# Kernel optimization log

Measured on AMD Instinct MI355X. Metric: run time of the kernel, lower is better.

The kernel has to match this reference:

```python
import jax, jax.numpy as jnp
import numpy as np

B, T, C, H = 2, 2048, 1024, 16
D = C // H  # head dim = 64


def setup_inputs() -> dict:
    key = jax.random.key(0)
    ks = jax.random.split(key, 3)
    x = jax.random.normal(ks[0], (B, T, C), dtype=jnp.float32)
    W_attn = jax.random.normal(ks[1], (C, 3 * C), dtype=jnp.float32) * (1.0 / np.sqrt(C))
    b_attn = jnp.zeros((3 * C,), dtype=jnp.float32)
    W_proj = jax.random.normal(ks[2], (C, C), dtype=jnp.float32) * (1.0 / np.sqrt(C))
    b_proj = jnp.zeros((C,), dtype=jnp.float32)
    return {"x": x, "W_attn": W_attn, "b_attn": b_attn, "W_proj": W_proj, "b_proj": b_proj}


def reference(x, W_attn, b_attn, W_proj, b_proj):
    Bb, Tt, Cc = x.shape
    qkv = x @ W_attn + b_attn                       # [B,T,3C]
    q, k, v = jnp.split(qkv, 3, axis=-1)            # each [B,T,C]
    q = q.reshape(Bb, Tt, H, D).transpose(0, 2, 1, 3)  # [B,H,T,D]
    k = k.reshape(Bb, Tt, H, D).transpose(0, 2, 1, 3)
    v = v.reshape(Bb, Tt, H, D).transpose(0, 2, 1, 3)
    # NOTE: original scales by 1/sqrt(n_embd), not 1/sqrt(head_dim)
    scale = 1.0 / np.sqrt(Cc)
    wei = jnp.einsum('bhqd,bhkd->bhqk', q, k) * scale  # [B,H,T,T]
    causal = jnp.tril(jnp.ones((Tt, Tt), dtype=bool))
    wei = jnp.where(causal, wei, -jnp.inf)
    wei = jax.nn.softmax(wei, axis=-1)
    out = jnp.einsum('bhqk,bhkd->bhqd', wei, v)        # [B,H,T,D]
    out = out.transpose(0, 2, 1, 3).reshape(Bb, Tt, Cc)
    return out @ W_proj + b_proj
```

## Files before the change

kernel.cpp:

```cpp
#include <hip/hip_runtime.h>


typedef short bfrag __attribute__((ext_vector_type(8)));
typedef float facc  __attribute__((ext_vector_type(4)));
typedef float f16v  __attribute__((ext_vector_type(16)));
typedef float f4v   __attribute__((ext_vector_type(4)));
typedef unsigned int u32x2 __attribute__((ext_vector_type(2)));
typedef unsigned int u32x4v __attribute__((ext_vector_type(4)));
typedef unsigned short u16;

#define MFMA16(a, b, c) __builtin_amdgcn_mfma_f32_16x16x32_bf16((a), (b), (c), 0, 0, 0)
#define MFMA32(a, b, c) __builtin_amdgcn_mfma_f32_32x32x16_bf16((a), (b), (c), 0, 0, 0)

__device__ __forceinline__ u16 f2bf(float f) {
  union { float f; unsigned u; } v; v.f = f;
  unsigned r = v.u + 0x7fffu + ((v.u >> 16) & 1u);
  return (u16)(r >> 16);
}

__device__ __forceinline__ unsigned cvtpk(float lo, float hi) {
  unsigned r;
  asm("v_cvt_pk_bf16_f32 %0, %1, %2" : "=v"(r) : "v"(lo), "v"(hi));
  return r;
}

__device__ __forceinline__ void async_lds16(const void* g, void* l) {
  __builtin_amdgcn_global_load_lds(
      (const __attribute__((address_space(1))) unsigned char*)g,
      (__attribute__((address_space(3))) unsigned char*)l, 16, 0, 0);
}


__global__ void cast_bf16_kernel(const float* __restrict__ s, u16* __restrict__ d, int n) {
  int i = (blockIdx.x * blockDim.x + threadIdx.x) * 4;
  if (i >= n) return;
  f4v v = *reinterpret_cast<const f4v*>(s + i);
  u32x2 w;
  w[0] = (unsigned)f2bf(v[0]) | ((unsigned)f2bf(v[1]) << 16);
  w[1] = (unsigned)f2bf(v[2]) | ((unsigned)f2bf(v[3]) << 16);
  *reinterpret_cast<u32x2*>(d + i) = w;
}

__global__ void transpose_cast_kernel(const float* __restrict__ src, u16* __restrict__ dst,
                                      int K, int N) {
  __shared__ float tile[32][33];
  int tx = threadIdx.x, ty = threadIdx.y;
  int n0 = blockIdx.x * 32, k0 = blockIdx.y * 32;
  for (int j = ty; j < 32; j += 8)
    tile[j][tx] = src[(size_t)(k0 + j) * N + (n0 + tx)];
  __syncthreads();
  for (int j = ty; j < 32; j += 8)
    dst[(size_t)(n0 + j) * K + (k0 + tx)] = f2bf(tile[tx][j]);
}


template <int EPI>
__global__ __launch_bounds__(256) void gemm_kernel(
    const u16* __restrict__ A, const u16* __restrict__ Bt,
    const float* __restrict__ bias, float* __restrict__ outf,
    u16* __restrict__ qb, u16* __restrict__ kb, u16* __restrict__ vb) {
  constexpr int KD = 1024;
  __shared__ u16 As[128 * 32];
  __shared__ u16 Bs[128 * 32];
  const int t = threadIdx.x;
  const int l = t & 63, w = t >> 6;
  const int wm = w >> 1, wn = w & 1;
  const int lg = l >> 4, lc = l & 15;
  const int m0 = blockIdx.y * 128, n0 = blockIdx.x * 128;
  facc acc[4][4] = {};
  const int srow = t >> 2, scol = (t & 3) * 8;
  const u16* ga = A + (size_t)(m0 + srow) * KD + scol;
  const u16* gb = Bt + (size_t)(n0 + srow) * KD + scol;
  u16* la0 = As + t * 8;  u16* la1 = As + 2048 + t * 8;
  u16* lb0 = Bs + t * 8;  u16* lb1 = Bs + 2048 + t * 8;
  for (int kt = 0; kt < KD / 32; ++kt) {
    __syncthreads();
    async_lds16(ga + kt * 32, la0);
    async_lds16(ga + 64 * KD + kt * 32, la1);
    async_lds16(gb + kt * 32, lb0);
    async_lds16(gb + 64 * KD + kt * 32, lb1);
    __syncthreads();
    bfrag a[4], b[4];
#pragma unroll
    for (int mi = 0; mi < 4; ++mi)
      a[mi] = *reinterpret_cast<const bfrag*>(As + (wm * 64 + mi * 16 + lc) * 32 + lg * 8);
#pragma unroll
    for (int ni = 0; ni < 4; ++ni)
      b[ni] = *reinterpret_cast<const bfrag*>(Bs + (wn * 64 + ni * 16 + lc) * 32 + lg * 8);
#pragma unroll
    for (int mi = 0; mi < 4; ++mi)
#pragma unroll
      for (int ni = 0; ni < 4; ++ni)
        acc[mi][ni] = MFMA16(a[mi], b[ni], acc[mi][ni]);
  }
#pragma unroll
  for (int mi = 0; mi < 4; ++mi) {
#pragma unroll
    for (int ni = 0; ni < 4; ++ni) {
#pragma unroll
      for (int r = 0; r < 4; ++r) {
        int gm = m0 + wm * 64 + mi * 16 + lg * 4 + r;
        int gn = n0 + wn * 64 + ni * 16 + lc;
        float val = acc[mi][ni][r] + bias[gn];
        if constexpr (EPI == 0) {
          int sec = gn >> 10, ci = gn & 1023;
          int h = ci >> 6, d = ci & 63;
          int b_ = gm >> 11, tq = gm & 2047;
          int bh = b_ * 16 + h;
          if (sec == 0) {
            qb[((size_t)bh * 2048 + tq) * 64 + d] = f2bf(val * 0.045084439f);
          } else if (sec == 1) {
            kb[((size_t)bh * 2048 + tq) * 64 + d] = f2bf(val);
          } else {
            vb[((size_t)bh * 64 + d) * 2048 + tq] = f2bf(val);
          }
        } else {
          outf[(size_t)gm * 1024 + gn] = val;
        }
      }
    }
  }
}


__global__ __launch_bounds__(128, 2) void attn_kernel(
    const u16* __restrict__ Qb, const u16* __restrict__ Kb,
    const u16* __restrict__ Vtb, u16* __restrict__ attn) {
  constexpr int T = 2048;
  __shared__ u16 Ks[2][64 * 64];
  const int t = threadIdx.x;
  const int l = t & 63, w = t >> 6;
  const int c = l & 31, h = l >> 5;
  const int b = blockIdx.x;
  const int bh = b & 31;
  const int tile = 31 - (b >> 5);
  const int ntile = tile + 1;
  const size_t base = (size_t)bh * T * 64;
  const u16* Qp = Qb + base;
  const u16* Kp = Kb + base;
  const u16* Vp = Vtb + base;
  const int q0 = tile * 64 + w * 32;

  bfrag qf[4];
#pragma unroll
  for (int dt = 0; dt < 4; ++dt)
    qf[dt] = *reinterpret_cast<const bfrag*>(Qp + (size_t)(q0 + c) * 64 + dt * 16 + 8 * h);

  f16v o[2] = {};
  f16v s[2];
  float m_ = -1e30f, l_ = 0.f;

  const int srow = w * 32 + (l >> 3);
  const int sw8  = ((t & 7) ^ ((t >> 3) & 7)) * 8;
  const int loff = w * 2048 + l * 8;

#define STAGE_K(bufi, kvb_)                                                      \
  {                                                                              \
    _Pragma("unroll")                                                            \
    for (int j = 0; j < 4; ++j)                                                  \
      async_lds16(Kp + (size_t)((kvb_) + srow + 8 * j) * 64 + sw8,               \
                  &Ks[bufi][loff + 512 * j]);                                    \
  }

#define LOADV(vf, kvb_)                                                          \
  {                                                                              \
    _Pragma("unroll")                                                            \
    for (int nt = 0; nt < 2; ++nt)                                               \
      _Pragma("unroll")                                                          \
      for (int k2 = 0; k2 < 4; ++k2)                                             \
        vf[nt * 4 + k2] = *reinterpret_cast<const bfrag*>(                       \
            Vp + (size_t)(32 * nt + c) * T + (kvb_) + 16 * k2 + 8 * h);          \
  }

  auto qk = [&](const u16* ks) {
    const f16v z = {};
    s[0] = z; s[1] = z;
    __builtin_amdgcn_s_setprio(1);
#pragma unroll
    for (int kt = 0; kt < 2; ++kt)
#pragma unroll
      for (int dt = 0; dt < 4; ++dt) {
        const bfrag a = *reinterpret_cast<const bfrag*>(
            ks + (32 * kt + c) * 64 + (((2 * dt + h) ^ (c & 7)) * 8));
        s[kt] = MFMA32(a, qf[dt], s[kt]);
      }
    __builtin_amdgcn_s_setprio(0);
  };

  auto pv = [&](const bfrag pa[4], const bfrag vf[8]) {
    __builtin_amdgcn_s_setprio(1);
#pragma unroll
    for (int nt = 0; nt < 2; ++nt)
#pragma unroll
      for (int k2 = 0; k2 < 4; ++k2)
        o[nt] = MFMA32(pa[k2], vf[nt * 4 + k2], o[nt]);
    __builtin_amdgcn_s_setprio(0);
  };

  auto softmax_pa = [&](int it, bfrag pa[4]) {
    if (it == ntile - 1) {
      const int kvb = 64 * it;
      const int qq = q0 + c;
#pragma unroll
      for (int kt = 0; kt < 2; ++kt)
#pragma unroll
        for (int r = 0; r < 16; ++r) {
          const int kk = kvb + 32 * kt + (r & 3) + 8 * (r >> 2) + 4 * h;
          if (kk > qq) s[kt][r] = -1e30f;
        }
    }
    float pms[4] = {-1e30f, -1e30f, -1e30f, -1e30f};
#pragma unroll
    for (int kt = 0; kt < 2; ++kt)
#pragma unroll
      for (int r = 0; r < 16; ++r) pms[r & 3] = fmaxf(pms[r & 3], s[kt][r]);
    float pm = fmaxf(fmaxf(pms[0], pms[1]), fmaxf(pms[2], pms[3]));
    pm = fmaxf(pm, __shfl_xor(pm, 32));
    if (!__all(pm <= m_ + 8.0f)) {
      const float mn = fmaxf(m_, pm);
      const float al = exp2f(m_ - mn);
      l_ *= al;
#pragma unroll
      for (int r = 0; r < 16; ++r) {
        const float ar = __shfl(al, (r & 3) + 8 * (r >> 2) + 4 * h);
        o[0][r] *= ar;
        o[1][r] *= ar;
      }
      m_ = mn;
    }
    float ps[4] = {0.f, 0.f, 0.f, 0.f};
#pragma unroll
    for (int kt = 0; kt < 2; ++kt)
#pragma unroll
      for (int r = 0; r < 16; ++r) {
        const float e = exp2f(s[kt][r] - m_);
        s[kt][r] = e;
        ps[r & 3] += e;
      }
    float pss = (ps[0] + ps[1]) + (ps[2] + ps[3]);
    pss += __shfl_xor(pss, 32);
    l_ += pss;
#pragma unroll
    for (int kt = 0; kt < 2; ++kt)
#pragma unroll
      for (int sub = 0; sub < 2; ++sub) {
        const int bs = 8 * sub;
        unsigned x1 = cvtpk(s[kt][bs + 0], s[kt][bs + 1]);
        unsigned y1 = cvtpk(s[kt][bs + 4], s[kt][bs + 5]);
        asm volatile("v_permlane32_swap_b32 %0, %1" : "+v"(x1), "+v"(y1));
        unsigned x2 = cvtpk(s[kt][bs + 2], s[kt][bs + 3]);
        unsigned y2 = cvtpk(s[kt][bs + 6], s[kt][bs + 7]);
        asm volatile("v_permlane32_swap_b32 %0, %1" : "+v"(x2), "+v"(y2));
        union { u32x4v wv; bfrag f; } u;
        u.wv[0] = x1; u.wv[1] = x2; u.wv[2] = y1; u.wv[3] = y2;
        pa[2 * kt + sub] = u.f;
      }
  };

  bfrag vfA[8], vfB[8], paA[4], paB[4];

  STAGE_K(0, 0);
  LOADV(vfA, 0);
  __syncthreads();
  if (ntile > 1) STAGE_K(1, 64);
  qk(Ks[0]);
  softmax_pa(0, paA);

  bool lastA = true;
  for (int it = 1; it < ntile; ) {
    __syncthreads();
    if (it + 1 < ntile) STAGE_K((it + 1) & 1, 64 * (it + 1));
    LOADV(vfB, 64 * it);
    qk(Ks[it & 1]);
    pv(paA, vfA);
    softmax_pa(it, paB);
    ++it; lastA = false;
    if (it >= ntile) break;
    __syncthreads();
    if (it + 1 < ntile) STAGE_K((it + 1) & 1, 64 * (it + 1));
    LOADV(vfA, 64 * it);
    qk(Ks[it & 1]);
    pv(paB, vfB);
    softmax_pa(it, paA);
    ++it; lastA = true;
  }
  if (lastA) pv(paA, vfA); else pv(paB, vfB);

  const int b_ = bh >> 4, hd = bh & 15;
  const float linv = 1.0f / l_;
#pragma unroll
  for (int r = 0; r < 16; ++r) {
    const int row = (r & 3) + 8 * (r >> 2) + 4 * h;
    const float lr = __shfl(linv, row);
    const int tq = q0 + row;
#pragma unroll
    for (int nt = 0; nt < 2; ++nt) {
      const int col = hd * 64 + 32 * nt + c;
      attn[((size_t)(b_ * T + tq)) * 1024 + col] = f2bf(o[nt][r] * lr);
    }
  }
#undef STAGE_K
#undef LOADV
}


extern "C" void kernel_launch(void* const* d_in, const int* in_sizes, int n_in,
                              void* d_out, int out_size, void* d_ws, size_t ws_size,
                              hipStream_t stream) {
  const float* x      = (const float*)d_in[0];
  const float* W_attn = (const float*)d_in[1];
  const float* b_attn = (const float*)d_in[2];
  const float* W_proj = (const float*)d_in[3];
  const float* b_proj = (const float*)d_in[4];
  float* out = (float*)d_out;
  char* ws = (char*)d_ws;
  u16* xb   = (u16*)(ws);
  u16* Wat  = (u16*)(ws + (8u  << 20));
  u16* Wpt  = (u16*)(ws + (14u << 20));
  u16* Qb   = (u16*)(ws + (16u << 20));
  u16* Kb   = (u16*)(ws + (24u << 20));
  u16* Vtb  = (u16*)(ws + (32u << 20));
  u16* attn = (u16*)(ws + (40u << 20));

  cast_bf16_kernel<<<4096, 256, 0, stream>>>(x, xb, 4096 * 1024);
  transpose_cast_kernel<<<dim3(96, 32), dim3(32, 8), 0, stream>>>(W_attn, Wat, 1024, 3072);
  transpose_cast_kernel<<<dim3(32, 32), dim3(32, 8), 0, stream>>>(W_proj, Wpt, 1024, 1024);
  gemm_kernel<0><<<dim3(24, 32), 256, 0, stream>>>(xb, Wat, b_attn, nullptr, Qb, Kb, Vtb);
  attn_kernel<<<1024, 128, 0, stream>>>(Qb, Kb, Vtb, attn);
  gemm_kernel<1><<<dim3(8, 32), 256, 0, stream>>>(attn, Wpt, b_proj, out, nullptr, nullptr, nullptr);
}
```

Baseline: 138.8 us.

## Use single-wave attention blocks loading K directly into registers without LDS

The attention kernel now launches one 64-thread wave per block, each covering 32 query rows, instead of two waves sharing a 64-row tile. K fragments are loaded straight from global memory into registers and prefetched one iteration ahead, replacing the double-buffered async LDS staging and its __syncthreads barriers. This removes LDS traffic and block synchronisation and doubles the number of blocks for scheduling. In exchange, K reuse between the two waves of a tile is lost, so K is read from global or L2 twice as often, and register pressure grows from holding K fragments.

After: 158.4 us. 1.14x slower.

```diff
diff --git a/kernel.cpp b/kernel.cpp
--- a/kernel.cpp
+++ b/kernel.cpp
@@ -123,23 +123,21 @@
 }
 
 
-__global__ __launch_bounds__(128, 2) void attn_kernel(
+__global__ __launch_bounds__(64, 2) void attn_kernel(
     const u16* __restrict__ Qb, const u16* __restrict__ Kb,
     const u16* __restrict__ Vtb, u16* __restrict__ attn) {
   constexpr int T = 2048;
-  __shared__ u16 Ks[2][64 * 64];
-  const int t = threadIdx.x;
-  const int l = t & 63, w = t >> 6;
+  const int l = threadIdx.x & 63;
   const int c = l & 31, h = l >> 5;
   const int b = blockIdx.x;
   const int bh = b & 31;
-  const int tile = 31 - (b >> 5);
-  const int ntile = tile + 1;
+  const int chunk = 63 - (b >> 5);
+  const int ntile = (chunk >> 1) + 1;
+  const int q0 = chunk * 32;
   const size_t base = (size_t)bh * T * 64;
   const u16* Qp = Qb + base;
   const u16* Kp = Kb + base;
   const u16* Vp = Vtb + base;
-  const int q0 = tile * 64 + w * 32;
 
   bfrag qf[4];
 #pragma unroll
@@ -150,18 +148,15 @@
   f16v s[2];
   float m_ = -1e30f, l_ = 0.f;
 
-  const int srow = w * 32 + (l >> 3);
-  const int sw8  = ((t & 7) ^ ((t >> 3) & 7)) * 8;
-  const int loff = w * 2048 + l * 8;
-
-#define STAGE_K(bufi, kvb_)                                                      \
+#define LOADK(kf, kvb_)                                                          \
   {                                                                              \
     _Pragma("unroll")                                                            \
-    for (int j = 0; j < 4; ++j)                                                  \
-      async_lds16(Kp + (size_t)((kvb_) + srow + 8 * j) * 64 + sw8,               \
-                  &Ks[bufi][loff + 512 * j]);                                    \
-  }
-
+    for (int kt = 0; kt < 2; ++kt)                                               \
+      _Pragma("unroll")                                                          \
+      for (int dt = 0; dt < 4; ++dt)                                             \
+        kf[kt * 4 + dt] = *reinterpret_cast<const bfrag*>(                       \
+            Kp + (size_t)((kvb_) + 32 * kt + c) * 64 + 16 * dt + 8 * h);         \
+  }
 #define LOADV(vf, kvb_)                                                          \
   {                                                                              \
     _Pragma("unroll")                                                            \
@@ -172,18 +167,15 @@
             Vp + (size_t)(32 * nt + c) * T + (kvb_) + 16 * k2 + 8 * h);          \
   }
 
-  auto qk = [&](const u16* ks) {
+  auto qk = [&](const bfrag kf[8]) {
     const f16v z = {};
     s[0] = z; s[1] = z;
     __builtin_amdgcn_s_setprio(1);
 #pragma unroll
     for (int kt = 0; kt < 2; ++kt)
 #pragma unroll
-      for (int dt = 0; dt < 4; ++dt) {
-        const bfrag a = *reinterpret_cast<const bfrag*>(
-            ks + (32 * kt + c) * 64 + (((2 * dt + h) ^ (c & 7)) * 8));
-        s[kt] = MFMA32(a, qf[dt], s[kt]);
-      }
+      for (int dt = 0; dt < 4; ++dt)
+        s[kt] = MFMA32(kf[kt * 4 + dt], qf[dt], s[kt]);
     __builtin_amdgcn_s_setprio(0);
   };
 
@@ -257,34 +249,27 @@
       }
   };
 
-  bfrag vfA[8], vfB[8], paA[4], paB[4];
-
-  STAGE_K(0, 0);
+  bfrag kf[8], vfA[8], vfB[8], pa[4];
+
+  LOADK(kf, 0);
   LOADV(vfA, 0);
-  __syncthreads();
-  if (ntile > 1) STAGE_K(1, 64);
-  qk(Ks[0]);
-  softmax_pa(0, paA);
-
-  bool lastA = true;
-  for (int it = 1; it < ntile; ) {
-    __syncthreads();
-    if (it + 1 < ntile) STAGE_K((it + 1) & 1, 64 * (it + 1));
-    LOADV(vfB, 64 * it);
-    qk(Ks[it & 1]);
-    pv(paA, vfA);
-    softmax_pa(it, paB);
-    ++it; lastA = false;
-    if (it >= ntile) break;
-    __syncthreads();
-    if (it + 1 < ntile) STAGE_K((it + 1) & 1, 64 * (it + 1));
-    LOADV(vfA, 64 * it);
-    qk(Ks[it & 1]);
-    pv(paB, vfB);
-    softmax_pa(it, paA);
-    ++it; lastA = true;
-  }
-  if (lastA) pv(paA, vfA); else pv(paB, vfB);
+
+  int it = 0;
+  bool useA = true;
+  while (true) {
+    qk(kf);
+    if (it + 1 < ntile) LOADK(kf, 64 * (it + 1));
+    softmax_pa(it, pa);
+    if (useA) {
+      if (it + 1 < ntile) LOADV(vfB, 64 * (it + 1));
+      pv(pa, vfA);
+    } else {
+      if (it + 1 < ntile) LOADV(vfA, 64 * (it + 1));
+      pv(pa, vfB);
+    }
+    useA = !useA;
+    if (++it >= ntile) break;
+  }
 
   const int b_ = bh >> 4, hd = bh & 15;
   const float linv = 1.0f / l_;
@@ -299,7 +284,7 @@
       attn[((size_t)(b_ * T + tq)) * 1024 + col] = f2bf(o[nt][r] * lr);
     }
   }
-#undef STAGE_K
+#undef LOADK
 #undef LOADV
 }
 
@@ -326,6 +311,6 @@
   transpose_cast_kernel<<<dim3(96, 32), dim3(32, 8), 0, stream>>>(W_attn, Wat, 1024, 3072);
   transpose_cast_kernel<<<dim3(32, 32), dim3(32, 8), 0, stream>>>(W_proj, Wpt, 1024, 1024);
   gemm_kernel<0><<<dim3(24, 32), 256, 0, stream>>>(xb, Wat, b_attn, nullptr, Qb, Kb, Vtb);
-  attn_kernel<<<1024, 128, 0, stream>>>(Qb, Kb, Vtb, attn);
+  attn_kernel<<<2048, 64, 0, stream>>>(Qb, Kb, Vtb, attn);
   gemm_kernel<1><<<dim3(8, 32), 256, 0, stream>>>(attn, Wpt, b_proj, out, nullptr, nullptr, nullptr);
 }
```

## Split KV range across two waves per query chunk and merge partial softmax

Applied to the files above, without the earlier changes.

The attention kernel now assigns each block a 32-row query chunk and has its two waves process alternating 64-key tiles, each keeping its own running max, sum and output. The partial results are then combined through shared memory using a flash-decoding style rescale. Grid size doubles to 2048 blocks, which gives more parallelism and better balance across the causal triangle. In exchange, the cross-tile software pipelining of QK and PV is lost, and the kernel adds an LDS reduction step and more K/V loads per query row.

Result: no change. 138.8 us (-0.0%).

```diff
diff --git a/kernel.cpp b/kernel.cpp
--- a/kernel.cpp
+++ b/kernel.cpp
@@ -127,19 +127,20 @@
     const u16* __restrict__ Qb, const u16* __restrict__ Kb,
     const u16* __restrict__ Vtb, u16* __restrict__ attn) {
   constexpr int T = 2048;
-  __shared__ u16 Ks[2][64 * 64];
+  __shared__ u16 Ks[2][2][64 * 64];
   const int t = threadIdx.x;
   const int l = t & 63, w = t >> 6;
   const int c = l & 31, h = l >> 5;
   const int b = blockIdx.x;
   const int bh = b & 31;
-  const int tile = 31 - (b >> 5);
-  const int ntile = tile + 1;
+  const int chunk = 63 - (b >> 5);
+  const int ntile = (chunk >> 1) + 1;
+  const int nrounds = (ntile + 1) >> 1;
+  const int q0 = chunk * 32;
   const size_t base = (size_t)bh * T * 64;
   const u16* Qp = Qb + base;
   const u16* Kp = Kb + base;
   const u16* Vp = Vtb + base;
-  const int q0 = tile * 64 + w * 32;
 
   bfrag qf[4];
 #pragma unroll
@@ -150,18 +151,18 @@
   f16v s[2];
   float m_ = -1e30f, l_ = 0.f;
 
-  const int srow = w * 32 + (l >> 3);
-  const int sw8  = ((t & 7) ^ ((t >> 3) & 7)) * 8;
-  const int loff = w * 2048 + l * 8;
-
-#define STAGE_K(bufi, kvb_)                                                      \
+  const int srow0 = l >> 3;
+  const int sw8   = ((l & 7) ^ (l >> 3)) * 8;
+  u16* kb0 = &Ks[0][w][0];
+  u16* kb1 = &Ks[1][w][0];
+
+#define STAGE_K(dst, kvb_)                                                       \
   {                                                                              \
     _Pragma("unroll")                                                            \
-    for (int j = 0; j < 4; ++j)                                                  \
-      async_lds16(Kp + (size_t)((kvb_) + srow + 8 * j) * 64 + sw8,               \
-                  &Ks[bufi][loff + 512 * j]);                                    \
-  }
-
+    for (int j = 0; j < 8; ++j)                                                  \
+      async_lds16(Kp + (size_t)((kvb_) + srow0 + 8 * j) * 64 + sw8,              \
+                  (dst) + 512 * j);                                              \
+  }
 #define LOADV(vf, kvb_)                                                          \
   {                                                                              \
     _Pragma("unroll")                                                            \
@@ -257,46 +258,57 @@
       }
   };
 
-  bfrag vfA[8], vfB[8], paA[4], paB[4];
-
-  STAGE_K(0, 0);
-  LOADV(vfA, 0);
+  bfrag vfA[8], vfB[8], pa[4];
+  if (w < ntile) { STAGE_K(kb0, 64 * w); LOADV(vfA, 64 * w); }
   __syncthreads();
-  if (ntile > 1) STAGE_K(1, 64);
-  qk(Ks[0]);
-  softmax_pa(0, paA);
-
-  bool lastA = true;
-  for (int it = 1; it < ntile; ) {
+  for (int r = 0; r < nrounds; ++r) {
+    const int it = 2 * r + w;
+    const int itn = it + 2;
+    if (itn < ntile) {
+      if (r & 1) { STAGE_K(kb0, 64 * itn); LOADV(vfA, 64 * itn); }
+      else       { STAGE_K(kb1, 64 * itn); LOADV(vfB, 64 * itn); }
+    }
+    if (it < ntile) {
+      qk((r & 1) ? kb1 : kb0);
+      softmax_pa(it, pa);
+      pv(pa, (r & 1) ? vfB : vfA);
+    }
     __syncthreads();
-    if (it + 1 < ntile) STAGE_K((it + 1) & 1, 64 * (it + 1));
-    LOADV(vfB, 64 * it);
-    qk(Ks[it & 1]);
-    pv(paA, vfA);
-    softmax_pa(it, paB);
-    ++it; lastA = false;
-    if (it >= ntile) break;
-    __syncthreads();
-    if (it + 1 < ntile) STAGE_K((it + 1) & 1, 64 * (it + 1));
-    LOADV(vfA, 64 * it);
-    qk(Ks[it & 1]);
-    pv(paB, vfB);
-    softmax_pa(it, paA);
-    ++it; lastA = true;
-  }
-  if (lastA) pv(paA, vfA); else pv(paB, vfB);
-
-  const int b_ = bh >> 4, hd = bh & 15;
-  const float linv = 1.0f / l_;
-#pragma unroll
-  for (int r = 0; r < 16; ++r) {
-    const int row = (r & 3) + 8 * (r >> 2) + 4 * h;
-    const float lr = __shfl(linv, row);
-    const int tq = q0 + row;
-#pragma unroll
-    for (int nt = 0; nt < 2; ++nt) {
-      const int col = hd * 64 + 32 * nt + c;
-      attn[((size_t)(b_ * T + tq)) * 1024 + col] = f2bf(o[nt][r] * lr);
+  }
+
+  float* Fo = (float*)&Ks[0][0][0];
+  float* Fm = Fo + 64 * 33;
+  float* Fl = Fm + 32;
+  if (w == 1) {
+#pragma unroll
+    for (int nt = 0; nt < 2; ++nt)
+#pragma unroll
+      for (int r = 0; r < 16; ++r) {
+        const int row = (r & 3) + 8 * (r >> 2) + 4 * h;
+        Fo[(nt * 32 + c) * 33 + row] = o[nt][r];
+      }
+    if (h == 0) { Fm[c] = m_; Fl[c] = l_; }
+  }
+  __syncthreads();
+  if (w == 0) {
+    const float m1v = Fm[c], l1v = Fl[c];
+    const float mm = fmaxf(m_, m1v);
+    const float a0 = exp2f(m_ - mm), a1 = exp2f(m1v - mm);
+    const float linv = 1.0f / (a0 * l_ + a1 * l1v);
+    const int b_ = bh >> 4, hd = bh & 15;
+#pragma unroll
+    for (int r = 0; r < 16; ++r) {
+      const int row = (r & 3) + 8 * (r >> 2) + 4 * h;
+      const float a0r = __shfl(a0, row);
+      const float a1r = __shfl(a1, row);
+      const float lr = __shfl(linv, row);
+      const int tq = q0 + row;
+#pragma unroll
+      for (int nt = 0; nt < 2; ++nt) {
+        const float o1 = Fo[(nt * 32 + c) * 33 + row];
+        attn[((size_t)(b_ * T + tq)) * 1024 + hd * 64 + 32 * nt + c] =
+            f2bf((a0r * o[nt][r] + a1r * o1) * lr);
+      }
     }
   }
 #undef STAGE_K
@@ -326,6 +338,6 @@
   transpose_cast_kernel<<<dim3(96, 32), dim3(32, 8), 0, stream>>>(W_attn, Wat, 1024, 3072);
   transpose_cast_kernel<<<dim3(32, 32), dim3(32, 8), 0, stream>>>(W_proj, Wpt, 1024, 1024);
   gemm_kernel<0><<<dim3(24, 32), 256, 0, stream>>>(xb, Wat, b_attn, nullptr, Qb, Kb, Vtb);
-  attn_kernel<<<1024, 128, 0, stream>>>(Qb, Kb, Vtb, attn);
+  attn_kernel<<<2048, 128, 0, stream>>>(Qb, Kb, Vtb, attn);
   gemm_kernel<1><<<dim3(8, 32), 256, 0, stream>>>(attn, Wpt, b_proj, out, nullptr, nullptr, nullptr);
 }
```
